# Optimization experiments

Hardware: AMD Instinct MI355X
Metric: run time of the kernel (lower is better)

## Reference

```python
import jax, jax.numpy as jnp
import numpy as np

B, T, D, H, W = 4, 2048, 256, 512, 32
EPS = 1e-5


def _xavier(key, fan_in, fan_out):
    # torch xavier_uniform on weight [out, in]; stored here as [in, out]
    limit = float(np.sqrt(6.0 / (fan_in + fan_out)))
    return jax.random.uniform(key, (fan_in, fan_out), jnp.float32, -limit, limit)


def _bias(key, fan_in, fan_out):
    # torch Linear default bias init: U(-1/sqrt(fan_in), 1/sqrt(fan_in))
    limit = float(1.0 / np.sqrt(fan_in))
    return jax.random.uniform(key, (fan_out,), jnp.float32, -limit, limit)


def setup_inputs() -> dict:
    key = jax.random.key(0)
    ks = jax.random.split(key, 16)
    inp = {
        "feature": jax.random.normal(ks[0], (B, T, D), jnp.float32),
        "gamma": jnp.ones((D,), jnp.float32),
        "beta": jnp.zeros((D,), jnp.float32),
        "w1": _xavier(ks[1], D, H), "b1": _bias(ks[2], D, H),
        "w2": _xavier(ks[3], H, H), "b2": _bias(ks[4], H, H),
        "w3": _xavier(ks[5], D, H), "b3": _bias(ks[6], H, H),
        "w4": _xavier(ks[7], H, H), "b4": _bias(ks[8], H, H),
        "w5": _xavier(ks[9], D, H), "b5": _bias(ks[10], H, H),
        "w6": _xavier(ks[11], H, H), "b6": _bias(ks[12], H, H),
        "window": W,
    }
    return inp


def reference(feature, gamma, beta, w1, b1, w2, b2, w3, b3, w4, b4, w5, b5, w6, b6, window):
    Bsz, Tlen, Din = feature.shape
    nb = Tlen // window
    x = feature.reshape(Bsz, nb, window, Din)  # [B, nb, W, D] window blocks

    # LayerNorm over last dim
    mu = jnp.mean(x, axis=-1, keepdims=True)
    var = jnp.mean((x - mu) ** 2, axis=-1, keepdims=True)
    n = (x - mu) * jax.lax.rsqrt(var + EPS) * gamma + beta

    Q = jnp.tanh(n @ w1 + b1) @ w2 + b2  # [B, nb, W, H]
    K = jnp.tanh(n @ w3 + b3) @ w4 + b4
    V = jax.nn.relu(n @ w5 + b5) @ w6 + b6

    Hdim = w2.shape[1]
    sqrt_feat = jnp.sqrt(jnp.float32(Hdim))
    sqrt_time = jnp.sqrt(jnp.float32(window))

    # time-axis attention: [B, nb, W, W]
    beta_time = jnp.einsum('bnwh,bnvh->bnwv', Q, K) / sqrt_feat
    # feature-axis attention: [B, nb, H, H]
    beta_feat = jnp.einsum('bnwh,bnwg->bnhg', Q, K) / sqrt_time

    A_time = jax.nn.softmax(beta_time, axis=-1)
    A_feat = jax.nn.softmax(beta_feat, axis=-2)

    feat = jnp.einsum('bnwh,bnhg->bnwg', V, A_feat)   # V @ A_feat
    out = jnp.einsum('bnwv,bnvg->bnwg', A_time, feat)  # A_time @ (V @ A_feat)
    return out.reshape(Bsz, Tlen, Hdim)
```

## Files before the change

### kernel.cpp

```cpp
#include <hip/hip_runtime.h>
#include <hip/hip_bf16.h>

typedef unsigned short u16;
typedef __attribute__((ext_vector_type(8))) unsigned short ushort8;
typedef __attribute__((ext_vector_type(8))) short short8;
typedef __attribute__((ext_vector_type(4))) float f32x4;
typedef __attribute__((ext_vector_type(4))) unsigned uint4_t;

#define DEV __device__ __forceinline__

DEV float b2f(u16 u){ return __uint_as_float(((unsigned)u) << 16); }
DEV u16 f2b(float f){
  unsigned x = __float_as_uint(f);
  return (u16)((x + 0x7fffu + ((x >> 16) & 1u)) >> 16);
}
DEV short8 ld8(const u16* p){ return __builtin_bit_cast(short8, *(const ushort8*)p); }
DEV f32x4 mfma(short8 a, short8 b, f32x4 c){
  return __builtin_amdgcn_mfma_f32_16x16x32_bf16(a, b, c, 0, 0, 0);
}
DEV float fast_tanh(float x){
  float e = __expf(2.f * x);
  return 1.f - 2.f / (e + 1.f);
}
DEV unsigned pk2(float lo, float hi){
  return (unsigned)f2b(lo) | ((unsigned)f2b(hi) << 16);
}

__global__ __launch_bounds__(256) void kt6(
    const float* __restrict__ w1, const float* __restrict__ w2,
    const float* __restrict__ w3, const float* __restrict__ w4,
    const float* __restrict__ w5, const float* __restrict__ w6,
    u16* __restrict__ ws)
{
  __shared__ u16 tile[64][72];
  const float* w; u16* wt; int K;
  switch (blockIdx.z) {
    case 0:  w = w1; wt = ws;          K = 256; break;
    case 1:  w = w2; wt = ws + 131072; K = 512; break;
    case 2:  w = w3; wt = ws + 393216; K = 256; break;
    case 3:  w = w4; wt = ws + 524288; K = 512; break;
    case 4:  w = w5; wt = ws + 786432; K = 256; break;
    default: w = w6; wt = ws + 917504; K = 512; break;
  }
  int k0 = blockIdx.y * 64;
  if (k0 >= K) return;
  int n0 = blockIdx.x * 64;
  int t = threadIdx.x;
  int r = t >> 2, c0 = (t & 3) * 16;
  const float* src = w + (size_t)(k0 + r) * 512 + n0 + c0;
  #pragma unroll
  for (int jj = 0; jj < 4; ++jj) {
    float4 v = *(const float4*)(src + jj * 4);
    tile[r][c0 + jj*4 + 0] = f2b(v.x);
    tile[r][c0 + jj*4 + 1] = f2b(v.y);
    tile[r][c0 + jj*4 + 2] = f2b(v.z);
    tile[r][c0 + jj*4 + 3] = f2b(v.w);
  }
  __syncthreads();
  ushort8 o0, o1;
  #pragma unroll
  for (int j = 0; j < 8; ++j) { o0[j] = tile[c0 + j][r]; o1[j] = tile[c0 + 8 + j][r]; }
  u16* dst = wt + (size_t)(n0 + r) * K + k0 + c0;
  *(ushort8*)dst       = o0;
  *(ushort8*)(dst + 8) = o1;
}


__global__ __launch_bounds__(256) void ln_k(
    const float* __restrict__ xg, const float* __restrict__ gg,
    const float* __restrict__ bgm, u16* __restrict__ ng)
{
  int row = blockIdx.x * 8 + (threadIdx.x >> 5);
  int l32 = threadIdx.x & 31;
  const float* xr = xg + (size_t)row*256 + l32*8;
  float xf[8];
  #pragma unroll
  for (int j = 0; j < 8; j += 4) {
    float4 v = *(const float4*)(xr + j);
    xf[j] = v.x; xf[j+1] = v.y; xf[j+2] = v.z; xf[j+3] = v.w;
  }
  float s = 0.f, ss = 0.f;
  #pragma unroll
  for (int j = 0; j < 8; ++j){ s += xf[j]; ss += xf[j]*xf[j]; }
  #pragma unroll
  for (int m = 1; m < 32; m <<= 1){ s += __shfl_xor(s, m); ss += __shfl_xor(ss, m); }
  float mean = s * (1.f/256.f);
  float var  = ss * (1.f/256.f) - mean*mean;
  float rs   = rsqrtf(var + 1e-5f);
  float gf[8], bf[8];
  #pragma unroll
  for (int j = 0; j < 8; j += 4) {
    float4 gv = *(const float4*)(gg  + l32*8 + j);
    float4 bv = *(const float4*)(bgm + l32*8 + j);
    gf[j] = gv.x; gf[j+1] = gv.y; gf[j+2] = gv.z; gf[j+3] = gv.w;
    bf[j] = bv.x; bf[j+1] = bv.y; bf[j+2] = bv.z; bf[j+3] = bv.w;
  }
  ushort8 o0;
  #pragma unroll
  for (int j = 0; j < 8; ++j)
    o0[j] = f2b((xf[j] - mean)*rs*gf[j] + bf[j]);
  *(ushort8*)(ng + (size_t)row*256 + l32*8) = o0;
}

template<int NS, int ACT>
__global__ __launch_bounds__(512, 4) void gemm_tile(
    const u16* __restrict__ Abase, size_t a_zstride,
    const u16* __restrict__ wst, int w_off0,
    const float* __restrict__ bz0, const float* __restrict__ bz1, const float* __restrict__ bz2,
    u16* __restrict__ Cbase)
{
  constexpr int KA = NS * 32;
  __shared__ __align__(16) u16 smA[2 * 5120];
  __shared__ __align__(16) u16 smB[2 * 5120];
  const int z = blockIdx.z;
  const u16* A = Abase + (size_t)z * a_zstride;
  const u16* W = wst + w_off0 + z * 393216;
  const float* bias = (z == 0) ? bz0 : ((z == 1) ? bz1 : bz2);
  u16* C = Cbase + (size_t)z * 4194304;
  const int M0 = blockIdx.x * 128, N0 = blockIdx.y * 128;
  const int tid = threadIdx.x;
  const int wv = tid >> 6, ln = tid & 63, q = ln >> 4, r16 = ln & 15;
  const int m0w = (wv >> 2) * 64, n0w = (wv & 3) * 32;
  const f32x4 Z = {0.f, 0.f, 0.f, 0.f};

  const int srow = tid >> 2, scq = (tid & 3) * 8;
  const u16* gA = A + (size_t)(M0 + srow) * KA + scq;
  const u16* gB = W + (size_t)(N0 + srow) * KA + scq;
  u16* dA = smA + srow * 40 + scq;
  u16* dB = smB + srow * 40 + scq;

  ushort8 rA[2], rB[2];
  rA[0] = *(const ushort8*)gA;
  rB[0] = *(const ushort8*)gB;
  *(ushort8*)dA = rA[0];
  *(ushort8*)dB = rB[0];
  if (NS > 1) { rA[1] = *(const ushort8*)(gA + 32); rB[1] = *(const ushort8*)(gB + 32); }
  __syncthreads();

  f32x4 acc[4][2];
  #pragma unroll
  for (int mf = 0; mf < 4; ++mf){ acc[mf][0] = Z; acc[mf][1] = Z; }

  #pragma unroll
  for (int kk = 0; kk < NS; ++kk) {
    const int cur = kk & 1;
    const u16* bufA = smA + cur * 5120;
    const u16* bufB = smB + cur * 5120;
    short8 aF[4], bF[2];
    #pragma unroll
    for (int mf = 0; mf < 4; ++mf) aF[mf] = ld8(bufA + (m0w + mf*16 + r16)*40 + q*8);
    #pragma unroll
    for (int nf = 0; nf < 2; ++nf) bF[nf] = ld8(bufB + (n0w + nf*16 + r16)*40 + q*8);
    #pragma unroll
    for (int mf = 0; mf < 4; ++mf)
      #pragma unroll
      for (int nf = 0; nf < 2; ++nf)
        acc[mf][nf] = mfma(aF[mf], bF[nf], acc[mf][nf]);
    if (kk + 1 < NS) {
      *(ushort8*)(dA + (cur ^ 1) * 5120) = rA[(kk + 1) & 1];
      *(ushort8*)(dB + (cur ^ 1) * 5120) = rB[(kk + 1) & 1];
    }
    if (kk + 2 < NS) {
      rA[kk & 1] = *(const ushort8*)(gA + (kk + 2) * 32);
      rB[kk & 1] = *(const ushort8*)(gB + (kk + 2) * 32);
    }
    __syncthreads();
  }

  #pragma unroll
  for (int nf = 0; nf < 2; ++nf) {
    int col = N0 + n0w + nf*16 + r16;
    float bs = bias[col];
    #pragma unroll
    for (int mf = 0; mf < 4; ++mf)
      #pragma unroll
      for (int i = 0; i < 4; ++i) {
        int row = M0 + m0w + mf*16 + q*4 + i;
        float v = acc[mf][nf][i] + bs;
        if (ACT == 0) v = fast_tanh(v);
        else if (ACT == 1) v = fmaxf(v, 0.f);
        else if (ACT == 3) v = (z == 2) ? fmaxf(v, 0.f) : fast_tanh(v);
        C[(size_t)row * 512 + col] = f2b(v);
      }
  }
}

#define AV   0
#define AQT  16640
#define AKT  37120
#define ABT  57600
#define AAT  59712
#define ASM_ELS 60992

__global__ __launch_bounds__(1024) void attn_k(
    const u16* __restrict__ QKVg, float* __restrict__ outg)
{
  __shared__ __align__(16) u16 sm[ASM_ELS];
  const int tid = threadIdx.x;
  const int bid = blockIdx.x;
  const int wv = tid >> 6, ln = tid & 63, q = ln >> 4, r16 = ln & 15;
  const f32x4 Z = {0.f, 0.f, 0.f, 0.f};
  const float RS512 = 0.04419417382415922f;
  const float C32L2 = 0.25500526676986233f;
  const u16* Qg = QKVg + (size_t)bid * 16384;
  const u16* Kg = QKVg + 4194304 + (size_t)bid * 16384;
  const u16* Vg = QKVg + 8388608 + (size_t)bid * 16384;

  float* btf = (float*)(sm + ABT);
  if (wv < 4) {
    int mt = wv >> 1, nt = wv & 1;
    f32x4 acc = Z;
    const u16* qb = Qg + (mt*16 + r16)*512;
    const u16* kb = Kg + (nt*16 + r16)*512;
    #pragma unroll
    for (int kk = 0; kk < 16; ++kk)
      acc = mfma(ld8(qb + kk*32 + q*8), ld8(kb + kk*32 + q*8), acc);
    #pragma unroll
    for (int i = 0; i < 4; ++i)
      btf[(mt*16 + q*4 + i)*33 + nt*16 + r16] = acc[i] * RS512;
  } else if (wv < 12) {
    int t1 = tid - 256;
    int row = t1 & 31, cb = (t1 >> 5) * 32;
    const u16* src = Qg + row*512 + cb;
    ushort8 v[4];
    #pragma unroll
    for (int jj = 0; jj < 4; ++jj) v[jj] = *(const ushort8*)(src + jj*8);
    #pragma unroll
    for (int jj = 0; jj < 4; ++jj)
      #pragma unroll
      for (int j = 0; j < 8; ++j)
        sm[AQT + (cb + jj*8 + j)*40 + row] = v[jj][j];
  } else {
    int t2 = tid - 768;
    int vrow = t2 >> 3, seg = (t2 & 7) * 64;
    const u16* src = Vg + vrow*512 + seg;
    #pragma unroll
    for (int jj = 0; jj < 8; ++jj)
      *(ushort8*)(sm + AV + vrow*520 + seg + jj*8) = *(const ushort8*)(src + jj*8);
  }
  __syncthreads();

  if (tid < 512) {
    int row = tid >> 4, v2 = tid & 15;
    float v0 = btf[row*33 + v2], v1 = btf[row*33 + v2 + 16];
    float m = fmaxf(v0, v1);
    #pragma unroll
    for (int msk = 1; msk < 16; msk <<= 1) m = fmaxf(m, __shfl_xor(m, msk));
    float e0 = __expf(v0 - m), e1 = __expf(v1 - m);
    float sum = e0 + e1;
    #pragma unroll
    for (int msk = 1; msk < 16; msk <<= 1) sum += __shfl_xor(sum, msk);
    float inv = 1.f / sum;
    sm[AAT + row*40 + v2]      = f2b(e0 * inv);
    sm[AAT + row*40 + v2 + 16] = f2b(e1 * inv);
  } else {
    int t2 = tid - 512;
    int row = t2 & 31, cb = (t2 >> 5) * 32;
    const u16* src = Kg + row*512 + cb;
    ushort8 v[4];
    #pragma unroll
    for (int jj = 0; jj < 4; ++jj) v[jj] = *(const ushort8*)(src + jj*8);
    #pragma unroll
    for (int jj = 0; jj < 4; ++jj)
      #pragma unroll
      for (int j = 0; j < 8; ++j)
        sm[AKT + (cb + jj*8 + j)*40 + row] = v[jj][j];
  }
  __syncthreads();

  {
    const int g0 = wv * 32;
    const bool hi32 = (ln >= 32);
    const bool qodd = (q & 1);
    f32x4 facc[2][2];
    facc[0][0]=Z; facc[0][1]=Z; facc[1][0]=Z; facc[1][1]=Z;
    float csum[2] = {0.f, 0.f};
    short8 bK[2];
    #pragma unroll
    for (int gt = 0; gt < 2; ++gt)
      bK[gt] = ld8(sm + AKT + (size_t)(g0 + gt*16 + r16)*40 + q*8);

    #pragma unroll 2
    for (int ht = 0; ht < 16; ++ht) {
      f32x4 sv[2][2];
      #pragma unroll
      for (int smi = 0; smi < 2; ++smi) {
        short8 aQ = ld8(sm + AQT + (ht*32 + smi*16 + r16)*40 + q*8);
        #pragma unroll
        for (int gt = 0; gt < 2; ++gt)
          sv[smi][gt] = mfma(aQ, bK[gt], Z);
      }
      unsigned D[2][4];
      #pragma unroll
      for (int gt = 0; gt < 2; ++gt) {
        float e[2][4];
        #pragma unroll
        for (int smi = 0; smi < 2; ++smi)
          #pragma unroll
          for (int i = 0; i < 4; ++i) {
            float ev = exp2f(sv[smi][gt][i] * C32L2);
            e[smi][i] = ev;
            csum[gt] += ev;
          }
        #pragma unroll
        for (int k = 0; k < 2; ++k) {
          unsigned w0 = pk2(e[0][2*k], e[0][2*k+1]);
          unsigned w1 = pk2(e[1][2*k], e[1][2*k+1]);
          unsigned Pw0 = (unsigned)__shfl_xor((int)w0, 32);
          unsigned Pw1 = (unsigned)__shfl_xor((int)w1, 32);
          unsigned x = hi32 ? Pw1 : w0;
          unsigned y = hi32 ? w1 : Pw0;
          unsigned xs = (unsigned)__shfl_xor((int)x, 16);
          unsigned ys = (unsigned)__shfl_xor((int)y, 16);
          D[gt][k]     = qodd ? ys : x;
          D[gt][k + 2] = qodd ? y  : xs;
        }
      }
      #pragma unroll
      for (int mt = 0; mt < 2; ++mt) {
        short8 aV = ld8(sm + AV + (mt*16 + r16)*520 + ht*32 + q*8);
        #pragma unroll
        for (int gt = 0; gt < 2; ++gt) {
          uint4_t dv = {D[gt][0], D[gt][1], D[gt][2], D[gt][3]};
          short8 bE = __builtin_bit_cast(short8, dv);
          facc[mt][gt] = mfma(aV, bE, facc[mt][gt]);
        }
      }
    }
    float inv[2];
    #pragma unroll
    for (int gt = 0; gt < 2; ++gt) {
      float cs = csum[gt];
      cs += __shfl_xor(cs, 16);
      cs += __shfl_xor(cs, 32);
      inv[gt] = 1.f / cs;
    }
    #pragma unroll
    for (int mt = 0; mt < 2; ++mt)
      #pragma unroll
      for (int gt = 0; gt < 2; ++gt)
        #pragma unroll
        for (int i = 0; i < 4; ++i) {
          int w = mt*16 + q*4 + i;
          int g = g0 + gt*16 + r16;
          sm[AKT + g*40 + w] = f2b(facc[mt][gt][i] * inv[gt]);
        }
  }

  {
    const int g0 = wv * 32;
    short8 aA0 = ld8(sm + AAT + r16*40 + q*8);
    short8 aA1 = ld8(sm + AAT + (16 + r16)*40 + q*8);
    #pragma unroll
    for (int gt = 0; gt < 2; ++gt) {
      short8 bF = ld8(sm + AKT + (size_t)(g0 + gt*16 + r16)*40 + q*8);
      f32x4 o0 = mfma(aA0, bF, Z);
      f32x4 o1 = mfma(aA1, bF, Z);
      #pragma unroll
      for (int i = 0; i < 4; ++i) {
        int g = g0 + gt*16 + r16;
        outg[(size_t)(bid*32 + q*4 + i)*512 + g]      = o0[i];
        outg[(size_t)(bid*32 + 16 + q*4 + i)*512 + g] = o1[i];
      }
    }
  }
}


#define OFF_V   0
#define OFF_N   16640
#define OFF_T   25088
#define OFF_Q   41728
#define OFF_K   58368
#define OFF_BT  75008
#define OFF_QT  16640
#define OFF_KT  37120
#define OFF_AT  78080
#define OFF_FT  37120
#define SMEM_ELS 79360

template<int ACT>
DEV void mlp_branch(const u16* __restrict__ nl, u16* __restrict__ tl, u16* __restrict__ ol,
                    const u16* __restrict__ wA, const float* __restrict__ bA,
                    const u16* __restrict__ wB, const float* __restrict__ bB,
                    int wv, int q, int r16)
{
  const f32x4 Z = {0.f, 0.f, 0.f, 0.f};
  const int c0 = wv*32 + r16;
  float biasA0 = bA[c0], biasA1 = bA[c0 + 16];
  float biasB0 = bB[c0], biasB1 = bB[c0 + 16];
  {
    const u16* cp0 = wA + (size_t)c0*256 + q*8;
    const u16* cp1 = cp0 + 16*256;
    const u16* a0p = nl + r16 * 264 + q*8;
    const u16* a1p = nl + (16 + r16) * 264 + q*8;
    f32x4 acc[2][2];
    acc[0][0]=Z; acc[0][1]=Z; acc[1][0]=Z; acc[1][1]=Z;
    #pragma unroll
    for (int kk = 0; kk < 8; ++kk) {
      short8 a0 = ld8(a0p + kk*32);
      short8 a1 = ld8(a1p + kk*32);
      short8 b0 = ld8(cp0 + kk*32);
      short8 b1 = ld8(cp1 + kk*32);
      acc[0][0] = mfma(a0, b0, acc[0][0]);
      acc[1][0] = mfma(a1, b0, acc[1][0]);
      acc[0][1] = mfma(a0, b1, acc[0][1]);
      acc[1][1] = mfma(a1, b1, acc[1][1]);
    }
    #pragma unroll
    for (int gt = 0; gt < 2; ++gt) {
      float bias = gt ? biasA1 : biasA0;
      #pragma unroll
      for (int mt = 0; mt < 2; ++mt)
        #pragma unroll
        for (int i = 0; i < 4; ++i) {
          float v = acc[mt][gt][i] + bias;
          v = (ACT == 0) ? fast_tanh(v) : fmaxf(v, 0.f);
          tl[(mt*16 + q*4 + i)*520 + c0 + gt*16] = f2b(v);
        }
    }
  }
  __syncthreads();
  {
    const u16* cp0 = wB + (size_t)c0*512 + q*8;
    const u16* cp1 = cp0 + 16*512;
    const u16* a0p = tl + r16 * 520 + q*8;
    const u16* a1p = tl + (16 + r16) * 520 + q*8;
    f32x4 acc[2][2];
    acc[0][0]=Z; acc[0][1]=Z; acc[1][0]=Z; acc[1][1]=Z;
    #pragma unroll
    for (int kk = 0; kk < 16; ++kk) {
      short8 a0 = ld8(a0p + kk*32);
      short8 a1 = ld8(a1p + kk*32);
      short8 b0 = ld8(cp0 + kk*32);
      short8 b1 = ld8(cp1 + kk*32);
      acc[0][0] = mfma(a0, b0, acc[0][0]);
      acc[1][0] = mfma(a1, b0, acc[1][0]);
      acc[0][1] = mfma(a0, b1, acc[0][1]);
      acc[1][1] = mfma(a1, b1, acc[1][1]);
    }
    #pragma unroll
    for (int gt = 0; gt < 2; ++gt) {
      float bias = gt ? biasB1 : biasB0;
      #pragma unroll
      for (int mt = 0; mt < 2; ++mt)
        #pragma unroll
        for (int i = 0; i < 4; ++i)
          ol[(mt*16 + q*4 + i)*520 + c0 + gt*16] = f2b(acc[mt][gt][i] + bias);
    }
  }
}

__global__ __launch_bounds__(1024) void fused_main(
    const float* __restrict__ xg, const float* __restrict__ gg, const float* __restrict__ bgm,
    const float* __restrict__ b1, const float* __restrict__ b2, const float* __restrict__ b3,
    const float* __restrict__ b4, const float* __restrict__ b5, const float* __restrict__ b6,
    const u16* __restrict__ wst, float* __restrict__ outg)
{
  __shared__ __align__(16) u16 sm[SMEM_ELS];
  const int tid = threadIdx.x;
  const int bid = blockIdx.x;
  const int wv = tid >> 6, ln = tid & 63, q = ln >> 4, r16 = ln & 15;
  const f32x4 Z = {0.f, 0.f, 0.f, 0.f};
  const float RS512 = 0.04419417382415922f;
  const float C32L2 = 0.25500526676986233f;

  {
    int row = tid >> 5, l32 = tid & 31;
    const float* xr = xg + (size_t)(bid*32 + row)*256 + l32*8;
    float xf[8];
    #pragma unroll
    for (int j = 0; j < 8; j += 4) {
      float4 v = *(const float4*)(xr + j);
      xf[j] = v.x; xf[j+1] = v.y; xf[j+2] = v.z; xf[j+3] = v.w;
    }
    float s = 0.f, ss = 0.f;
    #pragma unroll
    for (int j = 0; j < 8; ++j){ s += xf[j]; ss += xf[j]*xf[j]; }
    #pragma unroll
    for (int m = 1; m < 32; m <<= 1){ s += __shfl_xor(s, m); ss += __shfl_xor(ss, m); }
    float mean = s * (1.f/256.f);
    float var  = ss * (1.f/256.f) - mean*mean;
    float rs   = rsqrtf(var + 1e-5f);
    float gf[8], bf[8];
    #pragma unroll
    for (int j = 0; j < 8; j += 4) {
      float4 gv = *(const float4*)(gg  + l32*8 + j);
      float4 bv = *(const float4*)(bgm + l32*8 + j);
      gf[j] = gv.x; gf[j+1] = gv.y; gf[j+2] = gv.z; gf[j+3] = gv.w;
      bf[j] = bv.x; bf[j+1] = bv.y; bf[j+2] = bv.z; bf[j+3] = bv.w;
    }
    ushort8 o0;
    #pragma unroll
    for (int j = 0; j < 8; ++j)
      o0[j] = f2b((xf[j] - mean)*rs*gf[j] + bf[j]);
    *(ushort8*)(sm + OFF_N + row*264 + l32*8) = o0;
  }
  __syncthreads();

  mlp_branch<0>(sm+OFF_N, sm+OFF_T, sm+OFF_Q, wst,          b1, wst + 131072, b2, wv, q, r16);
  __syncthreads();
  mlp_branch<0>(sm+OFF_N, sm+OFF_T, sm+OFF_K, wst + 393216, b3, wst + 524288, b4, wv, q, r16);
  __syncthreads();
  mlp_branch<1>(sm+OFF_N, sm+OFF_T, sm+OFF_V, wst + 786432, b5, wst + 917504, b6, wv, q, r16);
  __syncthreads();

  float* btf = (float*)(sm + OFF_BT);
  if (wv < 4) {
    int mt = wv >> 1, nt = wv & 1;
    f32x4 acc = Z;
    const u16* qb = sm + OFF_Q + (mt*16 + r16)*520;
    const u16* kb = sm + OFF_K + (nt*16 + r16)*520;
    for (int kk = 0; kk < 16; ++kk)
      acc = mfma(ld8(qb + kk*32 + q*8), ld8(kb + kk*32 + q*8), acc);
    #pragma unroll
    for (int i = 0; i < 4; ++i)
      btf[(mt*16 + q*4 + i)*33 + nt*16 + r16] = acc[i] * RS512;
  } else if (wv < 12) {
    int t1 = tid - 256;
    int row = t1 & 31, cb = (t1 >> 5) * 32;
    const u16* src = sm + OFF_Q + row*520 + cb;
    ushort8 v[4];
    #pragma unroll
    for (int jj = 0; jj < 4; ++jj) v[jj] = *(const ushort8*)(src + jj*8);
    #pragma unroll
    for (int jj = 0; jj < 4; ++jj)
      #pragma unroll
      for (int j = 0; j < 8; ++j)
        sm[OFF_QT + (cb + jj*8 + j)*40 + row] = v[jj][j];
  }
  __syncthreads();

  if (tid < 512) {
    int row = tid >> 4, v2 = tid & 15;
    float v0 = btf[row*33 + v2], v1 = btf[row*33 + v2 + 16];
    float m = fmaxf(v0, v1);
    #pragma unroll
    for (int msk = 1; msk < 16; msk <<= 1) m = fmaxf(m, __shfl_xor(m, msk));
    float e0 = __expf(v0 - m), e1 = __expf(v1 - m);
    float sum = e0 + e1;
    #pragma unroll
    for (int msk = 1; msk < 16; msk <<= 1) sum += __shfl_xor(sum, msk);
    float inv = 1.f / sum;
    sm[OFF_AT + row*40 + v2]      = f2b(e0 * inv);
    sm[OFF_AT + row*40 + v2 + 16] = f2b(e1 * inv);
  } else {
    int t2 = tid - 512;
    int row = t2 & 31, cb = (t2 >> 5) * 32;
    const u16* src = sm + OFF_K + row*520 + cb;
    ushort8 v[4];
    #pragma unroll
    for (int jj = 0; jj < 4; ++jj) v[jj] = *(const ushort8*)(src + jj*8);
    #pragma unroll
    for (int jj = 0; jj < 4; ++jj)
      #pragma unroll
      for (int j = 0; j < 8; ++j)
        sm[OFF_KT + (cb + jj*8 + j)*40 + row] = v[jj][j];
  }
  __syncthreads();

  {
    const int g0 = wv * 32;
    const bool hi32 = (ln >= 32);
    const bool qodd = (q & 1);
    f32x4 facc[2][2];
    facc[0][0]=Z; facc[0][1]=Z; facc[1][0]=Z; facc[1][1]=Z;
    float csum[2] = {0.f, 0.f};
    short8 bK[2];
    #pragma unroll
    for (int gt = 0; gt < 2; ++gt)
      bK[gt] = ld8(sm + OFF_KT + (size_t)(g0 + gt*16 + r16)*40 + q*8);

    #pragma unroll 2
    for (int ht = 0; ht < 16; ++ht) {
      f32x4 sv[2][2];
      #pragma unroll
      for (int smi = 0; smi < 2; ++smi) {
        short8 aQ = ld8(sm + OFF_QT + (ht*32 + smi*16 + r16)*40 + q*8);
        #pragma unroll
        for (int gt = 0; gt < 2; ++gt)
          sv[smi][gt] = mfma(aQ, bK[gt], Z);
      }
      unsigned D[2][4];
      #pragma unroll
      for (int gt = 0; gt < 2; ++gt) {
        float e[2][4];
        #pragma unroll
        for (int smi = 0; smi < 2; ++smi)
          #pragma unroll
          for (int i = 0; i < 4; ++i) {
            float ev = exp2f(sv[smi][gt][i] * C32L2);
            e[smi][i] = ev;
            csum[gt] += ev;
          }
        #pragma unroll
        for (int k = 0; k < 2; ++k) {
          unsigned w0 = pk2(e[0][2*k], e[0][2*k+1]);
          unsigned w1 = pk2(e[1][2*k], e[1][2*k+1]);
          unsigned Pw0 = (unsigned)__shfl_xor((int)w0, 32);
          unsigned Pw1 = (unsigned)__shfl_xor((int)w1, 32);
          unsigned x = hi32 ? Pw1 : w0;
          unsigned y = hi32 ? w1 : Pw0;
          unsigned xs = (unsigned)__shfl_xor((int)x, 16);
          unsigned ys = (unsigned)__shfl_xor((int)y, 16);
          D[gt][k]     = qodd ? ys : x;
          D[gt][k + 2] = qodd ? y  : xs;
        }
      }
      #pragma unroll
      for (int mt = 0; mt < 2; ++mt) {
        short8 aV = ld8(sm + OFF_V + (mt*16 + r16)*520 + ht*32 + q*8);
        #pragma unroll
        for (int gt = 0; gt < 2; ++gt) {
          uint4_t dv = {D[gt][0], D[gt][1], D[gt][2], D[gt][3]};
          short8 bE = __builtin_bit_cast(short8, dv);
          facc[mt][gt] = mfma(aV, bE, facc[mt][gt]);
        }
      }
    }
    float inv[2];
    #pragma unroll
    for (int gt = 0; gt < 2; ++gt) {
      float cs = csum[gt];
      cs += __shfl_xor(cs, 16);
      cs += __shfl_xor(cs, 32);
      inv[gt] = 1.f / cs;
    }
    #pragma unroll
    for (int mt = 0; mt < 2; ++mt)
      #pragma unroll
      for (int gt = 0; gt < 2; ++gt)
        #pragma unroll
        for (int i = 0; i < 4; ++i) {
          int w = mt*16 + q*4 + i;
          int g = g0 + gt*16 + r16;
          sm[OFF_FT + g*40 + w] = f2b(facc[mt][gt][i] * inv[gt]);
        }
  }

  {
    const int g0 = wv * 32;
    short8 aA0 = ld8(sm + OFF_AT + r16*40 + q*8);
    short8 aA1 = ld8(sm + OFF_AT + (16 + r16)*40 + q*8);
    #pragma unroll
    for (int gt = 0; gt < 2; ++gt) {
      short8 bF = ld8(sm + OFF_FT + (size_t)(g0 + gt*16 + r16)*40 + q*8);
      f32x4 o0 = mfma(aA0, bF, Z);
      f32x4 o1 = mfma(aA1, bF, Z);
      #pragma unroll
      for (int i = 0; i < 4; ++i) {
        int g = g0 + gt*16 + r16;
        outg[(size_t)(bid*32 + q*4 + i)*512 + g]      = o0[i];
        outg[(size_t)(bid*32 + 16 + q*4 + i)*512 + g] = o1[i];
      }
    }
  }
}


extern "C" void kernel_launch(void* const* d_in, const int* in_sizes, int n_in,
                              void* d_out, int out_size, void* d_ws, size_t ws_size,
                              hipStream_t stream)
{
  const float* x  = (const float*)d_in[0];
  const float* gm = (const float*)d_in[1];
  const float* bt = (const float*)d_in[2];
  const float* w1 = (const float*)d_in[3];
  const float* b1 = (const float*)d_in[4];
  const float* w2 = (const float*)d_in[5];
  const float* b2 = (const float*)d_in[6];
  const float* w3 = (const float*)d_in[7];
  const float* b3 = (const float*)d_in[8];
  const float* w4 = (const float*)d_in[9];
  const float* b4 = (const float*)d_in[10];
  const float* w5 = (const float*)d_in[11];
  const float* b5 = (const float*)d_in[12];
  const float* w6 = (const float*)d_in[13];
  const float* b6 = (const float*)d_in[14];
  u16* ws  = (u16*)d_ws;
  float* out = (float*)d_out;

  const size_t WT_OFF  = 0;
  const size_t N_OFF   = 1179648;
  const size_t T_OFF   = 3276800;
  const size_t QKV_OFF = 15859712;
  const size_t NEED_BYTES = 28442624ULL * 2ULL;

  kt6<<<dim3(8, 8, 6), 256, 0, stream>>>(w1, w2, w3, w4, w5, w6, ws + WT_OFF);

  if (ws_size >= NEED_BYTES) {
    ln_k<<<1024, 256, 0, stream>>>(x, gm, bt, ws + N_OFF);
    gemm_tile<8, 3><<<dim3(64, 4, 3), 512, 0, stream>>>(
        ws + N_OFF, 0, ws + WT_OFF, 0, b1, b3, b5, ws + T_OFF);
    gemm_tile<16, 2><<<dim3(64, 4, 3), 512, 0, stream>>>(
        ws + T_OFF, 4194304, ws + WT_OFF, 131072, b2, b4, b6, ws + QKV_OFF);
    attn_k<<<256, 1024, 0, stream>>>(ws + QKV_OFF, out);
  } else {
    fused_main<<<256, 1024, 0, stream>>>(x, gm, bt, b1, b2, b3, b4, b5, b6, ws + WT_OFF, out);
  }
}
```

Before: 87.55 us.

## Merge weight prep with layernorm, stage GEMM stores via LDS, keep attention output in registers

Combines the weight transpose and layernorm kernels into one launch, which removes one kernel launch and lets the two jobs run side by side. The GEMM epilogue now writes the output tile to shared memory and then stores coalesced 16-byte rows instead of scattered 2-byte stores. In attention, the Q/K transposes pack pairs of rows into 32-bit LDS writes, and the normalized feature result is shuffled in registers straight into MFMA operands instead of taking an LDS round trip. Float-to-bf16 conversion uses the hardware packed convert instruction, whose rounding may differ slightly from the manual round-to-nearest-even code.

```diff
diff --git a/kernel.cpp b/kernel.cpp
--- a/kernel.cpp
+++ b/kernel.cpp
@@ -14,6 +14,11 @@
   unsigned x = __float_as_uint(f);
   return (u16)((x + 0x7fffu + ((x >> 16) & 1u)) >> 16);
 }
+DEV unsigned cvtpk(float lo, float hi){
+  unsigned r;
+  asm("v_cvt_pk_bf16_f32 %0, %1, %2" : "=v"(r) : "v"(lo), "v"(hi));
+  return r;
+}
 DEV short8 ld8(const u16* p){ return __builtin_bit_cast(short8, *(const ushort8*)p); }
 DEV f32x4 mfma(short8 a, short8 b, f32x4 c){
   return __builtin_amdgcn_mfma_f32_16x16x32_bf16(a, b, c, 0, 0, 0);
@@ -26,80 +31,81 @@
   return (unsigned)f2b(lo) | ((unsigned)f2b(hi) << 16);
 }
 
-__global__ __launch_bounds__(256) void kt6(
+__global__ __launch_bounds__(256) void prep_k(
     const float* __restrict__ w1, const float* __restrict__ w2,
     const float* __restrict__ w3, const float* __restrict__ w4,
     const float* __restrict__ w5, const float* __restrict__ w6,
-    u16* __restrict__ ws)
-{
-  __shared__ u16 tile[64][72];
-  const float* w; u16* wt; int K;
-  switch (blockIdx.z) {
-    case 0:  w = w1; wt = ws;          K = 256; break;
-    case 1:  w = w2; wt = ws + 131072; K = 512; break;
-    case 2:  w = w3; wt = ws + 393216; K = 256; break;
-    case 3:  w = w4; wt = ws + 524288; K = 512; break;
-    case 4:  w = w5; wt = ws + 786432; K = 256; break;
-    default: w = w6; wt = ws + 917504; K = 512; break;
-  }
-  int k0 = blockIdx.y * 64;
-  if (k0 >= K) return;
-  int n0 = blockIdx.x * 64;
-  int t = threadIdx.x;
-  int r = t >> 2, c0 = (t & 3) * 16;
-  const float* src = w + (size_t)(k0 + r) * 512 + n0 + c0;
-  #pragma unroll
-  for (int jj = 0; jj < 4; ++jj) {
-    float4 v = *(const float4*)(src + jj * 4);
-    tile[r][c0 + jj*4 + 0] = f2b(v.x);
-    tile[r][c0 + jj*4 + 1] = f2b(v.y);
-    tile[r][c0 + jj*4 + 2] = f2b(v.z);
-    tile[r][c0 + jj*4 + 3] = f2b(v.w);
-  }
-  __syncthreads();
-  ushort8 o0, o1;
-  #pragma unroll
-  for (int j = 0; j < 8; ++j) { o0[j] = tile[c0 + j][r]; o1[j] = tile[c0 + 8 + j][r]; }
-  u16* dst = wt + (size_t)(n0 + r) * K + k0 + c0;
-  *(ushort8*)dst       = o0;
-  *(ushort8*)(dst + 8) = o1;
-}
-
-
-__global__ __launch_bounds__(256) void ln_k(
+    u16* __restrict__ ws,
     const float* __restrict__ xg, const float* __restrict__ gg,
     const float* __restrict__ bgm, u16* __restrict__ ng)
 {
-  int row = blockIdx.x * 8 + (threadIdx.x >> 5);
-  int l32 = threadIdx.x & 31;
-  const float* xr = xg + (size_t)row*256 + l32*8;
-  float xf[8];
-  #pragma unroll
-  for (int j = 0; j < 8; j += 4) {
-    float4 v = *(const float4*)(xr + j);
-    xf[j] = v.x; xf[j+1] = v.y; xf[j+2] = v.z; xf[j+3] = v.w;
-  }
-  float s = 0.f, ss = 0.f;
-  #pragma unroll
-  for (int j = 0; j < 8; ++j){ s += xf[j]; ss += xf[j]*xf[j]; }
-  #pragma unroll
-  for (int m = 1; m < 32; m <<= 1){ s += __shfl_xor(s, m); ss += __shfl_xor(ss, m); }
-  float mean = s * (1.f/256.f);
-  float var  = ss * (1.f/256.f) - mean*mean;
-  float rs   = rsqrtf(var + 1e-5f);
-  float gf[8], bf[8];
-  #pragma unroll
-  for (int j = 0; j < 8; j += 4) {
-    float4 gv = *(const float4*)(gg  + l32*8 + j);
-    float4 bv = *(const float4*)(bgm + l32*8 + j);
-    gf[j] = gv.x; gf[j+1] = gv.y; gf[j+2] = gv.z; gf[j+3] = gv.w;
-    bf[j] = bv.x; bf[j+1] = bv.y; bf[j+2] = bv.z; bf[j+3] = bv.w;
-  }
-  ushort8 o0;
-  #pragma unroll
-  for (int j = 0; j < 8; ++j)
-    o0[j] = f2b((xf[j] - mean)*rs*gf[j] + bf[j]);
-  *(ushort8*)(ng + (size_t)row*256 + l32*8) = o0;
+  __shared__ u16 tile[64][72];
+  const int bid = blockIdx.x;
+  if (bid < 384) {
+    const int z = bid / 64, rem = bid % 64, by = rem / 8, bx = rem % 8;
+    const float* w; u16* wt; int K;
+    switch (z) {
+      case 0:  w = w1; wt = ws;          K = 256; break;
+      case 1:  w = w2; wt = ws + 131072; K = 512; break;
+      case 2:  w = w3; wt = ws + 393216; K = 256; break;
+      case 3:  w = w4; wt = ws + 524288; K = 512; break;
+      case 4:  w = w5; wt = ws + 786432; K = 256; break;
+      default: w = w6; wt = ws + 917504; K = 512; break;
+    }
+    int k0 = by * 64;
+    if (k0 >= K) return;
+    int n0 = bx * 64;
+    int t = threadIdx.x;
+    int r = t >> 2, c0 = (t & 3) * 16;
+    const float* src = w + (size_t)(k0 + r) * 512 + n0 + c0;
+    #pragma unroll
+    for (int jj = 0; jj < 4; ++jj) {
+      float4 v = *(const float4*)(src + jj * 4);
+      unsigned* tp = (unsigned*)&tile[r][c0 + jj*4];
+      tp[0] = cvtpk(v.x, v.y);
+      tp[1] = cvtpk(v.z, v.w);
+    }
+    __syncthreads();
+    ushort8 o0, o1;
+    #pragma unroll
+    for (int j = 0; j < 8; ++j) { o0[j] = tile[c0 + j][r]; o1[j] = tile[c0 + 8 + j][r]; }
+    u16* dst = wt + (size_t)(n0 + r) * K + k0 + c0;
+    *(ushort8*)dst       = o0;
+    *(ushort8*)(dst + 8) = o1;
+  } else {
+    const int lb = bid - 384;
+    int row = lb * 8 + (threadIdx.x >> 5);
+    int l32 = threadIdx.x & 31;
+    const float* xr = xg + (size_t)row*256 + l32*8;
+    float xf[8];
+    #pragma unroll
+    for (int j = 0; j < 8; j += 4) {
+      float4 v = *(const float4*)(xr + j);
+      xf[j] = v.x; xf[j+1] = v.y; xf[j+2] = v.z; xf[j+3] = v.w;
+    }
+    float s = 0.f, ss = 0.f;
+    #pragma unroll
+    for (int j = 0; j < 8; ++j){ s += xf[j]; ss += xf[j]*xf[j]; }
+    #pragma unroll
+    for (int m = 1; m < 32; m <<= 1){ s += __shfl_xor(s, m); ss += __shfl_xor(ss, m); }
+    float mean = s * (1.f/256.f);
+    float var  = ss * (1.f/256.f) - mean*mean;
+    float rs   = rsqrtf(var + 1e-5f);
+    float r8[8];
+    #pragma unroll
+    for (int j = 0; j < 8; j += 4) {
+      float4 gv = *(const float4*)(gg  + l32*8 + j);
+      float4 bv = *(const float4*)(bgm + l32*8 + j);
+      r8[j]   = (xf[j]   - mean)*rs*gv.x + bv.x;
+      r8[j+1] = (xf[j+1] - mean)*rs*gv.y + bv.y;
+      r8[j+2] = (xf[j+2] - mean)*rs*gv.z + bv.z;
+      r8[j+3] = (xf[j+3] - mean)*rs*gv.w + bv.w;
+    }
+    uint4_t o;
+    o[0] = cvtpk(r8[0], r8[1]); o[1] = cvtpk(r8[2], r8[3]);
+    o[2] = cvtpk(r8[4], r8[5]); o[3] = cvtpk(r8[6], r8[7]);
+    *(uint4_t*)(ng + (size_t)row*256 + l32*8) = o;
+  }
 }
 
 template<int NS, int ACT>
@@ -110,8 +116,9 @@
     u16* __restrict__ Cbase)
 {
   constexpr int KA = NS * 32;
-  __shared__ __align__(16) u16 smA[2 * 5120];
-  __shared__ __align__(16) u16 smB[2 * 5120];
+  __shared__ __align__(16) u16 sm[20480];
+  u16* smA = sm;
+  u16* smB = sm + 10240;
   const int z = blockIdx.z;
   const u16* A = Abase + (size_t)z * a_zstride;
   const u16* W = wst + w_off0 + z * 393216;
@@ -167,21 +174,29 @@
     __syncthreads();
   }
 
+  u16* ct = sm;
   #pragma unroll
   for (int nf = 0; nf < 2; ++nf) {
-    int col = N0 + n0w + nf*16 + r16;
-    float bs = bias[col];
+    int colL = n0w + nf*16 + r16;
+    float bs = bias[N0 + colL];
     #pragma unroll
     for (int mf = 0; mf < 4; ++mf)
       #pragma unroll
       for (int i = 0; i < 4; ++i) {
-        int row = M0 + m0w + mf*16 + q*4 + i;
+        int row = m0w + mf*16 + q*4 + i;
         float v = acc[mf][nf][i] + bs;
-        if (ACT == 0) v = fast_tanh(v);
-        else if (ACT == 1) v = fmaxf(v, 0.f);
+        if (ACT == 1) v = fmaxf(v, 0.f);
         else if (ACT == 3) v = (z == 2) ? fmaxf(v, 0.f) : fast_tanh(v);
-        C[(size_t)row * 512 + col] = f2b(v);
-      }
+        ct[row*132 + colL] = f2b(v);
+      }
+  }
+  __syncthreads();
+  #pragma unroll
+  for (int j = 0; j < 4; ++j) {
+    int row = (tid >> 4) + j*32;
+    int cb2 = (tid & 15) * 8;
+    ushort8 vv = *(const ushort8*)(ct + row*132 + cb2);
+    *(ushort8*)(C + (size_t)(M0 + row)*512 + N0 + cb2) = vv;
   }
 }
 
@@ -220,16 +235,18 @@
       btf[(mt*16 + q*4 + i)*33 + nt*16 + r16] = acc[i] * RS512;
   } else if (wv < 12) {
     int t1 = tid - 256;
-    int row = t1 & 31, cb = (t1 >> 5) * 32;
-    const u16* src = Qg + row*512 + cb;
-    ushort8 v[4];
-    #pragma unroll
-    for (int jj = 0; jj < 4; ++jj) v[jj] = *(const ushort8*)(src + jj*8);
-    #pragma unroll
-    for (int jj = 0; jj < 4; ++jj)
-      #pragma unroll
-      for (int j = 0; j < 8; ++j)
-        sm[AQT + (cb + jj*8 + j)*40 + row] = v[jj][j];
+    int rp = t1 & 15;
+    int cb = (t1 >> 4) * 16;
+    const u16* s0 = Qg + (2*rp)*512 + cb;
+    const u16* s1 = s0 + 512;
+    ushort8 a0 = *(const ushort8*)s0, a1 = *(const ushort8*)(s0 + 8);
+    ushort8 c0v = *(const ushort8*)s1, c1v = *(const ushort8*)(s1 + 8);
+    unsigned* qt32 = (unsigned*)(sm + AQT);
+    #pragma unroll
+    for (int j = 0; j < 8; ++j) {
+      qt32[(cb + j)*20 + rp]     = (unsigned)a0[j] | ((unsigned)c0v[j] << 16);
+      qt32[(cb + 8 + j)*20 + rp] = (unsigned)a1[j] | ((unsigned)c1v[j] << 16);
+    }
   } else {
     int t2 = tid - 768;
     int vrow = t2 >> 3, seg = (t2 & 7) * 64;
@@ -254,17 +271,19 @@
     sm[AAT + row*40 + v2]      = f2b(e0 * inv);
     sm[AAT + row*40 + v2 + 16] = f2b(e1 * inv);
   } else {
-    int t2 = tid - 512;
-    int row = t2 & 31, cb = (t2 >> 5) * 32;
-    const u16* src = Kg + row*512 + cb;
-    ushort8 v[4];
-    #pragma unroll
-    for (int jj = 0; jj < 4; ++jj) v[jj] = *(const ushort8*)(src + jj*8);
-    #pragma unroll
-    for (int jj = 0; jj < 4; ++jj)
-      #pragma unroll
-      for (int j = 0; j < 8; ++j)
-        sm[AKT + (cb + jj*8 + j)*40 + row] = v[jj][j];
+    int t1 = tid - 512;
+    int rp = t1 & 15;
+    int cb = (t1 >> 4) * 16;
+    const u16* s0 = Kg + (2*rp)*512 + cb;
+    const u16* s1 = s0 + 512;
+    ushort8 a0 = *(const ushort8*)s0, a1 = *(const ushort8*)(s0 + 8);
+    ushort8 c0v = *(const ushort8*)s1, c1v = *(const ushort8*)(s1 + 8);
+    unsigned* kt32 = (unsigned*)(sm + AKT);
+    #pragma unroll
+    for (int j = 0; j < 8; ++j) {
+      kt32[(cb + j)*20 + rp]     = (unsigned)a0[j] | ((unsigned)c0v[j] << 16);
+      kt32[(cb + 8 + j)*20 + rp] = (unsigned)a1[j] | ((unsigned)c1v[j] << 16);
+    }
   }
   __syncthreads();
 
@@ -304,8 +323,8 @@
           }
         #pragma unroll
         for (int k = 0; k < 2; ++k) {
-          unsigned w0 = pk2(e[0][2*k], e[0][2*k+1]);
-          unsigned w1 = pk2(e[1][2*k], e[1][2*k+1]);
+          unsigned w0 = cvtpk(e[0][2*k], e[0][2*k+1]);
+          unsigned w1 = cvtpk(e[1][2*k], e[1][2*k+1]);
           unsigned Pw0 = (unsigned)__shfl_xor((int)w0, 32);
           unsigned Pw1 = (unsigned)__shfl_xor((int)w1, 32);
           unsigned x = hi32 ? Pw1 : w0;
@@ -335,25 +354,35 @@
       cs += __shfl_xor(cs, 32);
       inv[gt] = 1.f / cs;
     }
-    #pragma unroll
-    for (int mt = 0; mt < 2; ++mt)
-      #pragma unroll
-      for (int gt = 0; gt < 2; ++gt)
-        #pragma unroll
-        for (int i = 0; i < 4; ++i) {
-          int w = mt*16 + q*4 + i;
-          int g = g0 + gt*16 + r16;
-          sm[AKT + g*40 + w] = f2b(facc[mt][gt][i] * inv[gt]);
-        }
-  }
-
-  {
-    const int g0 = wv * 32;
+    unsigned F[2][4];
+    #pragma unroll
+    for (int gt = 0; gt < 2; ++gt) {
+      float e0n[4], e1n[4];
+      #pragma unroll
+      for (int i = 0; i < 4; ++i) {
+        e0n[i] = facc[0][gt][i] * inv[gt];
+        e1n[i] = facc[1][gt][i] * inv[gt];
+      }
+      #pragma unroll
+      for (int k = 0; k < 2; ++k) {
+        unsigned w0 = cvtpk(e0n[2*k], e0n[2*k+1]);
+        unsigned w1 = cvtpk(e1n[2*k], e1n[2*k+1]);
+        unsigned Pw0 = (unsigned)__shfl_xor((int)w0, 32);
+        unsigned Pw1 = (unsigned)__shfl_xor((int)w1, 32);
+        unsigned x = hi32 ? Pw1 : w0;
+        unsigned y = hi32 ? w1 : Pw0;
+        unsigned xs = (unsigned)__shfl_xor((int)x, 16);
+        unsigned ys = (unsigned)__shfl_xor((int)y, 16);
+        F[gt][k]     = qodd ? ys : x;
+        F[gt][k + 2] = qodd ? y  : xs;
+      }
+    }
     short8 aA0 = ld8(sm + AAT + r16*40 + q*8);
     short8 aA1 = ld8(sm + AAT + (16 + r16)*40 + q*8);
     #pragma unroll
     for (int gt = 0; gt < 2; ++gt) {
-      short8 bF = ld8(sm + AKT + (size_t)(g0 + gt*16 + r16)*40 + q*8);
+      uint4_t fv = {F[gt][0], F[gt][1], F[gt][2], F[gt][3]};
+      short8 bF = __builtin_bit_cast(short8, fv);
       f32x4 o0 = mfma(aA0, bF, Z);
       f32x4 o1 = mfma(aA1, bF, Z);
       #pragma unroll
@@ -686,16 +715,17 @@
   const size_t QKV_OFF = 15859712;
   const size_t NEED_BYTES = 28442624ULL * 2ULL;
 
-  kt6<<<dim3(8, 8, 6), 256, 0, stream>>>(w1, w2, w3, w4, w5, w6, ws + WT_OFF);
-
   if (ws_size >= NEED_BYTES) {
-    ln_k<<<1024, 256, 0, stream>>>(x, gm, bt, ws + N_OFF);
+    prep_k<<<1408, 256, 0, stream>>>(w1, w2, w3, w4, w5, w6, ws + WT_OFF,
+                                     x, gm, bt, ws + N_OFF);
     gemm_tile<8, 3><<<dim3(64, 4, 3), 512, 0, stream>>>(
         ws + N_OFF, 0, ws + WT_OFF, 0, b1, b3, b5, ws + T_OFF);
     gemm_tile<16, 2><<<dim3(64, 4, 3), 512, 0, stream>>>(
         ws + T_OFF, 4194304, ws + WT_OFF, 131072, b2, b4, b6, ws + QKV_OFF);
     attn_k<<<256, 1024, 0, stream>>>(ws + QKV_OFF, out);
   } else {
+    prep_k<<<384, 256, 0, stream>>>(w1, w2, w3, w4, w5, w6, ws + WT_OFF,
+                                    x, gm, bt, ws + WT_OFF );
     fused_main<<<256, 1024, 0, stream>>>(x, gm, bt, b1, b2, b3, b4, b5, b6, ws + WT_OFF, out);
   }
 }
```

Result: faster. 83.75 us (-4.3%).
